# Kernel tuning notes

Hardware: AMD Instinct MI355X
Metric: run time of the kernel (lower is better)

## Reference

```python
import jax, jax.numpy as jnp
import numpy as np
import math

SEQ = 45000
FEAT = 30
DEPTH, HEADS, DK, MLP, C = 4, 4, 32, 512, 32
MAXSEQ = 512


def pos_embed_table():
    # Enformer-style basis functions over distances [-SEQ+1, SEQ-1]
    d = jnp.arange(-SEQ + 1, SEQ, dtype=jnp.float32)
    a = jnp.abs(d)[:, None]
    nb = FEAT // 6  # basis per class (exponential / central-mask / gamma)
    # exponential decay
    hl = 2.0 ** jnp.linspace(3.0, math.log(SEQ) / math.log(2.0), nb)
    e1 = jnp.exp(-math.log(2.0) / hl[None, :] * a)
    # central mask
    cw = 2.0 ** jnp.arange(1, nb + 1, dtype=jnp.float32) - 1.0
    e2 = (cw[None, :] > a).astype(jnp.float32)
    # gamma pdf
    stddev = SEQ / (2 * nb)
    start_mean = SEQ / nb
    mean = jnp.linspace(start_mean, float(SEQ), nb)
    conc = (mean / stddev) ** 2
    rate = mean / stddev ** 2
    logp = jax.scipy.special.xlogy(conc - 1.0, a) - rate * a
    logz = jax.scipy.special.gammaln(conc) - conc * jnp.log(rate)
    p = jnp.exp(logp - logz) + 1e-8
    e3 = p / jnp.max(p)
    e = jnp.concatenate([e1, e2, e3], axis=-1)
    return jnp.concatenate([e, jnp.sign(d)[:, None] * e], axis=-1)  # [2*SEQ-1, FEAT]


def layernorm(x, g, b, eps=1e-5):
    mu = jnp.mean(x, axis=-1, keepdims=True)
    var = jnp.var(x, axis=-1, keepdims=True)
    return (x - mu) * jax.lax.rsqrt(var + eps) * g + b


def setup_inputs() -> dict:
    key = jax.random.key(0)
    ks = jax.random.split(key, 16)
    B, L = 2, SEQ
    HD = HEADS * DK
    s = 0.02
    return {
        "x_skip": jax.random.normal(ks[0], (B, C, L), jnp.float32),
        "attention": jax.random.uniform(ks[1], (B, 3, L), jnp.float32),
        "ln1_g": jnp.ones((DEPTH, C), jnp.float32),
        "ln1_b": jnp.zeros((DEPTH, C), jnp.float32),
        "Wq": jax.random.normal(ks[2], (DEPTH, C, HD), jnp.float32) * s,
        "Wk": jax.random.normal(ks[3], (DEPTH, C, HD), jnp.float32) * s,
        "Wv": jax.random.normal(ks[4], (DEPTH, C, HD), jnp.float32) * s,
        "Wrel": jax.random.normal(ks[5], (DEPTH, FEAT, HD), jnp.float32) * s,
        "rcb": jax.random.normal(ks[6], (DEPTH, HEADS, DK), jnp.float32),
        "rpb": jax.random.normal(ks[7], (DEPTH, HEADS, DK), jnp.float32),
        "Wo": jax.random.normal(ks[8], (DEPTH, HD, C), jnp.float32) * s,
        "bo": jnp.zeros((DEPTH, C), jnp.float32),
        "ln2_g": jnp.ones((DEPTH, C), jnp.float32),
        "ln2_b": jnp.zeros((DEPTH, C), jnp.float32),
        "W1": jax.random.normal(ks[9], (DEPTH, C, MLP), jnp.float32) * s,
        "b1": jnp.zeros((DEPTH, MLP), jnp.float32),
        "W2": jax.random.normal(ks[10], (DEPTH, MLP, C), jnp.float32) * s,
        "b2": jnp.zeros((DEPTH, C), jnp.float32),
    }


def reference(x_skip, attention, ln1_g, ln1_b, Wq, Wk, Wv, Wrel, rcb, rpb, Wo, bo, ln2_g, ln2_b, W1, b1, W2, b2):
    B, Cc, L = x_skip.shape
    half = MAXSEQ // 2
    x_emb = jnp.swapaxes(x_skip, 1, 2)  # [B, L, C]
    # top splice sites by acceptor / donor score
    acc = jnp.argsort(-attention[:, 1, :], axis=1)[:, :half]
    don = jnp.argsort(-attention[:, 2, :], axis=1)[:, :half]
    idx = jnp.sort(jnp.concatenate([acc, don], axis=1), axis=1)  # [B, n]
    n = idx.shape[1]
    diff = idx[:, :, None] - idx[:, None, :] + SEQ - 1  # [B, n, n]
    positions = pos_embed_table()[diff]  # [B, n, n, FEAT]
    emb = jnp.take_along_axis(x_emb, idx[:, :, None], axis=1)  # [B, n, C]
    scale = DK ** -0.5
    for l in range(DEPTH):
        h = layernorm(emb, ln1_g[l], ln1_b[l])
        q = (h @ Wq[l]).reshape(B, n, HEADS, DK).transpose(0, 2, 1, 3) * scale
        k = (h @ Wk[l]).reshape(B, n, HEADS, DK).transpose(0, 2, 1, 3)
        v = (h @ Wv[l]).reshape(B, n, HEADS, DK).transpose(0, 2, 1, 3)
        content = jnp.einsum('bhid,bhjd->bhij', q + rcb[l][None, :, None, :], k)
        rel_k = (positions @ Wrel[l]).reshape(B, n, n, HEADS, DK)  # b i j h d
        rel = jnp.einsum('bhid,bijhd->bhij', q + rpb[l][None, :, None, :], rel_k)
        attn_w = jax.nn.softmax(content + rel, axis=-1)
        o = jnp.einsum('bhij,bhjd->bhid', attn_w, v)
        o = o.transpose(0, 2, 1, 3).reshape(B, n, HEADS * DK)
        emb = emb + o @ Wo[l] + bo[l]
        h2 = layernorm(emb, ln2_g[l], ln2_b[l])
        emb = emb + jax.nn.gelu(h2 @ W1[l] + b1[l], approximate=False) @ W2[l] + b2[l]
    out = jnp.zeros_like(x_emb).at[jnp.arange(B)[:, None], idx].set(emb)
    return jnp.swapaxes(out, 1, 2)  # [B, C, L]
```

## Files before the change

### kernel.cpp

```cpp
#include <hip/hip_runtime.h>
#include <math.h>

#define SEQL   45000
#define NBAT   2
#define CCH    32
#define NSEL   512
#define NHEAD  4
#define DKD    32
#define HDD    128
#define MLPD   512
#define CDCAP  2048
#define ETB    176

__device__ __forceinline__ unsigned short f2bf(float x) {
  unsigned u = __float_as_uint(x);
  u = (u + 0x7fffu + ((u >> 16) & 1u)) >> 16;
  return (unsigned short)u;
}
#define BFL(u) __uint_as_float((u) << 16)
#define BFH(u) __uint_as_float((u) & 0xffff0000u)
#define U8F(w, s) ((float)(((w) >> (s)) & 0xffu))

__global__ __launch_bounds__(256) void prep_kernel(unsigned char* __restrict__ E,
                                                   float* __restrict__ out) {
  {
    int nthr = gridDim.x * 256;
    int gt = blockIdx.x * 256 + threadIdx.x;
    float4 z4 = make_float4(0.f, 0.f, 0.f, 0.f);
    float4* o4 = (float4*)out;
    for (int i = gt; i < NBAT * CCH * SEQL / 4; i += nthr) o4[i] = z4;
  }
  if (blockIdx.x >= ETB) return;
  int a = blockIdx.x * 256 + threadIdx.x;
  if (a >= SEQL) return;
  float ad = (float)a;
  float outv[16];
  float log2S = log2f((float)SEQL);
  #pragma unroll
  for (int k = 0; k < 5; ++k) {
    float hl = exp2f(3.0f + (float)k * (log2S - 3.0f) * 0.25f);
    outv[k] = exp2f(-ad / hl);
  }
  const int cw[5] = {1, 3, 7, 15, 31};
  #pragma unroll
  for (int k = 0; k < 5; ++k) outv[5 + k] = (a < cw[k]) ? 1.0f : 0.0f;
  float pmax = 0.0f;
  float pk[5];
  #pragma unroll
  for (int k = 0; k < 5; ++k) {
    float mean = 9000.0f * (float)(k + 1);
    float sd = 4500.0f;
    float cc = (mean / sd) * (mean / sd);
    float rr = mean / (sd * sd);
    float logz = lgammaf(cc) - cc * logf(rr);
    float pp;
    if (a == 0) pp = 1e-8f;
    else pp = expf((cc - 1.0f) * logf(ad) - rr * ad - logz) + 1e-8f;
    pk[k] = pp;
    float mstar = (cc - 1.0f) / rr;
    float m0 = floorf(mstar), m1 = m0 + 1.0f;
    if (m1 > (float)(SEQL - 1)) m1 = (float)(SEQL - 1);
    float p0 = expf((cc - 1.0f) * logf(m0) - rr * m0 - logz) + 1e-8f;
    float p1 = expf((cc - 1.0f) * logf(m1) - rr * m1 - logz) + 1e-8f;
    pmax = fmaxf(pmax, fmaxf(p0, p1));
  }
  #pragma unroll
  for (int k = 0; k < 5; ++k) outv[10 + k] = pk[k] / pmax;
  outv[15] = 0.0f;
  unsigned by[16];
  #pragma unroll
  for (int k = 0; k < 15; ++k)
    by[k] = (unsigned)(fminf(fmaxf(outv[k], 0.f), 1.f) * 255.f + 0.5f);
  by[15] = 0u;
  uint4 o;
  o.x = by[0]  | (by[1]  << 8) | (by[2]  << 16) | (by[3]  << 24);
  o.y = by[4]  | (by[5]  << 8) | (by[6]  << 16) | (by[7]  << 24);
  o.z = by[8]  | (by[9]  << 8) | (by[10] << 16) | (by[11] << 24);
  o.w = by[12] | (by[13] << 8) | (by[14] << 16);
  *(uint4*)(E + (size_t)a * 16) = o;
}

__global__ __launch_bounds__(1024) void topk_channel_kernel(
    const float* __restrict__ att, unsigned* __restrict__ chsel) {
  __shared__ unsigned long long sc[CDCAP];
  __shared__ int hist[256];
  __shared__ int scan[256];
  __shared__ int aux[2];
  __shared__ int cnt;
  int ch4 = blockIdx.x, t = threadIdx.x;
  int b = ch4 >> 1, ch = ch4 & 1;
  const float* row = att + ((size_t)b * 3 + 1 + ch) * SEQL;
  if (t < 256) hist[t] = 0;
  if (t == 0) cnt = 0;
  __syncthreads();
  for (int i = t; i < SEQL; i += 1024)
    atomicAdd(&hist[__float_as_uint(row[i]) >> 24], 1);
  __syncthreads();
  if (t < 256) scan[t] = hist[t];
  __syncthreads();
  for (int d = 1; d < 256; d <<= 1) {
    int v = 0;
    if (t < 256) v = scan[t] + ((t + d < 256) ? scan[t + d] : 0);
    __syncthreads();
    if (t < 256) scan[t] = v;
    __syncthreads();
  }
  if (t < 256) {
    int sufEx = (t == 255) ? 0 : scan[t + 1];
    if (scan[t] >= 256 && sufEx < 256) { aux[0] = t; aux[1] = 256 - sufEx; }
  }
  __syncthreads();
  int B = aux[0], want = aux[1];
  if (t < 256) hist[t] = 0;
  __syncthreads();
  for (int i = t; i < SEQL; i += 1024) {
    unsigned key = __float_as_uint(row[i]);
    if ((int)(key >> 24) == B) atomicAdd(&hist[(key >> 16) & 0xffu], 1);
  }
  __syncthreads();
  if (t < 256) scan[t] = hist[t];
  __syncthreads();
  for (int d = 1; d < 256; d <<= 1) {
    int v = 0;
    if (t < 256) v = scan[t] + ((t + d < 256) ? scan[t + d] : 0);
    __syncthreads();
    if (t < 256) scan[t] = v;
    __syncthreads();
  }
  if (t < 256) {
    int sufEx = (t == 255) ? 0 : scan[t + 1];
    if (scan[t] >= want && sufEx < want) aux[0] = (B << 8) | t;
  }
  __syncthreads();
  unsigned T16 = (unsigned)aux[0];
  for (int i = t; i < SEQL; i += 1024) {
    unsigned key = __float_as_uint(row[i]);
    if ((key >> 16) >= T16) {
      int p = atomicAdd(&cnt, 1);
      if (p < CDCAP)
        sc[p] = ((unsigned long long)key << 32) | (unsigned)(~(unsigned)i);
    }
  }
  __syncthreads();
  int n = cnt; if (n > CDCAP) n = CDCAP;
  int P = 256;
  while (P < n) P <<= 1;
  for (int i2 = t; i2 < P; i2 += 1024)
    if (i2 >= n) sc[i2] = 0ull;
  __syncthreads();
  for (int k = 2; k <= P; k <<= 1) {
    for (int j = k >> 1; j > 0; j >>= 1) {
      for (int i2 = t; i2 < P; i2 += 1024) {
        int ixj = i2 ^ j;
        if (ixj > i2) {
          unsigned long long va = sc[i2], vb2 = sc[ixj];
          bool up = ((i2 & k) == 0);
          if ((va < vb2) == up) { sc[i2] = vb2; sc[ixj] = va; }
        }
      }
      __syncthreads();
    }
  }
  if (t < 256)
    chsel[(size_t)ch4 * 256 + t] = ~(unsigned)(sc[t] & 0xFFFFFFFFull);
}

__global__ __launch_bounds__(512) void topk_merge_kernel(const unsigned* __restrict__ chsel,
                                                         int* __restrict__ idx) {
  __shared__ int m[512];
  int b = blockIdx.x, tid = threadIdx.x;
  m[tid] = (int)chsel[(size_t)b * 512 + tid];
  __syncthreads();
  for (int k = 2; k <= 512; k <<= 1) {
    for (int j = k >> 1; j > 0; j >>= 1) {
      int ixj = tid ^ j;
      if (ixj > tid) {
        int va = m[tid], vb2 = m[ixj];
        bool up = ((tid & k) == 0);
        if ((va > vb2) == up) { m[tid] = vb2; m[ixj] = va; }
      }
      __syncthreads();
    }
  }
  idx[b * 512 + tid] = m[tid];
}

__global__ __launch_bounds__(128) void gqkv0_kernel(
    const float* __restrict__ x, const int* __restrict__ idx,
    const float* __restrict__ ln_g, const float* __restrict__ ln_b,
    const float* __restrict__ Wq, const float* __restrict__ Wk,
    const float* __restrict__ Wv, const float* __restrict__ Wrel,
    const float* __restrict__ rcb, const float* __restrict__ rpb,
    float* __restrict__ emb, float* __restrict__ qc,
    unsigned short* __restrict__ kbT, unsigned short* __restrict__ vT,
    float* __restrict__ wb) {
  __shared__ float qs[128];
  const int l = 0;
  int hd = threadIdx.x;
  int hh = hd >> 5, d = hd & 31;
  int row = blockIdx.x;
  int b = row >> 9, ii = row & 511;
  int li = idx[b * NSEL + ii];
  float h[32];
  float mu = 0.f;
  #pragma unroll
  for (int c = 0; c < 32; ++c) {
    h[c] = x[((size_t)b * CCH + c) * SEQL + li];
    mu += h[c];
  }
  if (hd < 32) emb[(size_t)row * CCH + hd] = h[hd];
  mu *= (1.0f / 32.0f);
  float var = 0.f;
  #pragma unroll
  for (int c = 0; c < 32; ++c) { float dd0 = h[c] - mu; var += dd0 * dd0; }
  var *= (1.0f / 32.0f);
  float rstd = rsqrtf(var + 1e-5f);
  const float* g = ln_g + l * CCH;
  const float* bb = ln_b + l * CCH;
  #pragma unroll
  for (int c = 0; c < 32; ++c) h[c] = (h[c] - mu) * rstd * g[c] + bb[c];
  const float* wq = Wq + (size_t)l * CCH * HDD + hd;
  const float* wk = Wk + (size_t)l * CCH * HDD + hd;
  const float* wv = Wv + (size_t)l * CCH * HDD + hd;
  float q = 0.f, kk = 0.f, vv = 0.f;
  #pragma unroll
  for (int c = 0; c < 32; ++c) {
    q += h[c] * wq[c * HDD];
    kk += h[c] * wk[c * HDD];
    vv += h[c] * wv[c * HDD];
  }
  q *= 0.17677669529663687f;
  qs[hd] = q;
  qc[(size_t)row * HDD + hd] = q + rcb[(l * NHEAD + hh) * DKD + d];
  size_t tpos = ((size_t)(b * 4 + hh) * 4 + (d >> 3)) * 4096 + (size_t)ii * 8 + (d & 7);
  kbT[tpos] = f2bf(kk);
  vT[tpos]  = f2bf(vv);
  __syncthreads();
  if (hd < 120) {
    int h2 = hd / 30, f = hd % 30;
    const float* wr = Wrel + ((size_t)l * 30 + f) * HDD + h2 * DKD;
    const float* rp = rpb + (l * NHEAD + h2) * DKD;
    const float* qsh = qs + h2 * DKD;
    float acc = 0.f;
    #pragma unroll
    for (int dd = 0; dd < 32; ++dd) acc += (qsh[dd] + rp[dd]) * wr[dd];
    wb[((size_t)row * NHEAD + h2) * 32 + f] = acc;
  }
}

__global__ __launch_bounds__(256, 4) void layer_kernel(
    const float* __restrict__ qc, const unsigned short* __restrict__ kbT,
    const unsigned short* __restrict__ vT, const float* __restrict__ wbuf,
    const unsigned char* __restrict__ E, const int* __restrict__ idx,
    const float* __restrict__ Wo, const float* __restrict__ bo,
    const float* __restrict__ ln2_g, const float* __restrict__ ln2_b,
    const float* __restrict__ W1, const float* __restrict__ b1,
    const float* __restrict__ W2, const float* __restrict__ b2,
    const float* __restrict__ ln1_g, const float* __restrict__ ln1_b,
    const float* __restrict__ Wq, const float* __restrict__ Wk,
    const float* __restrict__ Wv, const float* __restrict__ Wrel,
    const float* __restrict__ rcb, const float* __restrict__ rpb,
    float* __restrict__ emb, float* __restrict__ qcN,
    unsigned short* __restrict__ kbTN, unsigned short* __restrict__ vTN,
    float* __restrict__ wbN, float* __restrict__ out, int layer) {
  __shared__ float2 es2[8 * 512];
  __shared__ float obs[128];
  __shared__ float part[8][32];
  __shared__ float res[32];
  __shared__ float hln[32];
  __shared__ float fin[32];
  __shared__ float a1s[MLPD];
  __shared__ float qs[128];
  int bid = blockIdx.x;
  int b = bid >> 9;
  int i = bid & 511;
  int tid = threadIdx.x;
  int pos = idx[b * NSEL + i];
  #pragma unroll
  for (int rep = 0; rep < 2; ++rep) {
    int j = tid + rep * 256;
    int dj = pos - idx[b * NSEL + j];
    int a = dj < 0 ? -dj : dj;
    uint4 e = *(const uint4*)(E + (size_t)a * 16);
    float sgn = dj > 0 ? 1.f : (dj < 0 ? -1.f : 0.f);
    es2[0 * 512 + j] = make_float2(U8F(e.x, 0),  U8F(e.x, 8));
    es2[1 * 512 + j] = make_float2(U8F(e.x, 16), U8F(e.x, 24));
    es2[2 * 512 + j] = make_float2(U8F(e.y, 0),  U8F(e.y, 8));
    es2[3 * 512 + j] = make_float2(U8F(e.y, 16), U8F(e.y, 24));
    es2[4 * 512 + j] = make_float2(U8F(e.z, 0),  U8F(e.z, 8));
    es2[5 * 512 + j] = make_float2(U8F(e.z, 16), U8F(e.z, 24));
    es2[6 * 512 + j] = make_float2(U8F(e.w, 0),  U8F(e.w, 8));
    es2[7 * 512 + j] = make_float2(U8F(e.w, 16), sgn);
  }
  __syncthreads();
  {
    int h = tid >> 6, ln = tid & 63;
    const float* qrow = qc + (size_t)(b * NSEL + i) * HDD + h * DKD;
    float q[32];
    #pragma unroll
    for (int d4 = 0; d4 < 8; ++d4) {
      float4 qv = *(const float4*)(qrow + d4 * 4);
      q[d4 * 4 + 0] = qv.x; q[d4 * 4 + 1] = qv.y;
      q[d4 * 4 + 2] = qv.z; q[d4 * 4 + 3] = qv.w;
    }
    const float* wrow = wbuf + ((size_t)(b * NSEL + i) * NHEAD + h) * 32;
    float w0[15], w1[15];
    #pragma unroll
    for (int f = 0; f < 15; ++f) {
      w0[f] = wrow[f] * (1.0f / 255.0f);
      w1[f] = wrow[15 + f] * (1.0f / 255.0f);
    }
    const uint4* kb4 = (const uint4*)kbT + (size_t)(b * 4 + h) * 4 * 512;
    const uint4* vb4 = (const uint4*)vT + (size_t)(b * 4 + h) * 4 * 512;
    float lg[8];
    #pragma unroll
    for (int u = 0; u < 8; ++u) {
      int j = u * 64 + ln;
      float cacc = 0.f;
      #pragma unroll
      for (int dp = 0; dp < 4; ++dp) {
        uint4 kv = kb4[dp * 512 + j];
        cacc += q[dp * 8 + 0] * BFL(kv.x) + q[dp * 8 + 1] * BFH(kv.x)
              + q[dp * 8 + 2] * BFL(kv.y) + q[dp * 8 + 3] * BFH(kv.y)
              + q[dp * 8 + 4] * BFL(kv.z) + q[dp * 8 + 5] * BFH(kv.z)
              + q[dp * 8 + 6] * BFL(kv.w) + q[dp * 8 + 7] * BFH(kv.w);
      }
      float r0 = 0.f, r1 = 0.f;
      float2 e7 = es2[7 * 512 + j];
      #pragma unroll
      for (int f2 = 0; f2 < 7; ++f2) {
        float2 ee = es2[f2 * 512 + j];
        r0 += ee.x * w0[2 * f2] + ee.y * w0[2 * f2 + 1];
        r1 += ee.x * w1[2 * f2] + ee.y * w1[2 * f2 + 1];
      }
      r0 += e7.x * w0[14];
      r1 += e7.x * w1[14];
      lg[u] = cacc + r0 + e7.y * r1;
    }
    float m = lg[0];
    #pragma unroll
    for (int u = 1; u < 8; ++u) m = fmaxf(m, lg[u]);
    #pragma unroll
    for (int s = 1; s < 64; s <<= 1) m = fmaxf(m, __shfl_xor(m, s));
    float ssum = 0.f;
    #pragma unroll
    for (int u = 0; u < 8; ++u) { lg[u] = __expf(lg[u] - m); ssum += lg[u]; }
    #pragma unroll
    for (int s = 1; s < 64; s <<= 1) ssum += __shfl_xor(ssum, s);
    float invs = 1.0f / ssum;
    #pragma unroll
    for (int dp = 0; dp < 4; ++dp) {
      float acc[8] = {0.f, 0.f, 0.f, 0.f, 0.f, 0.f, 0.f, 0.f};
      #pragma unroll
      for (int u = 0; u < 8; ++u) {
        uint4 vv = vb4[dp * 512 + u * 64 + ln];
        float p = lg[u];
        acc[0] += p * BFL(vv.x); acc[1] += p * BFH(vv.x);
        acc[2] += p * BFL(vv.y); acc[3] += p * BFH(vv.y);
        acc[4] += p * BFL(vv.z); acc[5] += p * BFH(vv.z);
        acc[6] += p * BFL(vv.w); acc[7] += p * BFH(vv.w);
      }
      #pragma unroll
      for (int s = 1; s < 8; s <<= 1) {
        #pragma unroll
        for (int t = 0; t < 8; ++t) acc[t] += __shfl_xor(acc[t], s);
      }
      int sel = ln & 7;
      float y = acc[0];
      #pragma unroll
      for (int t = 1; t < 8; ++t) y = (sel == t) ? acc[t] : y;
      #pragma unroll
      for (int s = 8; s < 64; s <<= 1) y += __shfl_xor(y, s);
      if (ln < 8) obs[h * DKD + dp * 8 + ln] = y * invs;
    }
  }
  __syncthreads();
  int c = tid & 31, seg = tid >> 5;
  {
    const float* wo = Wo + (size_t)layer * HDD * CCH + c;
    float pacc = 0.f;
    #pragma unroll
    for (int k = 0; k < 16; ++k) {
      int kk = seg * 16 + k;
      pacc += obs[kk] * wo[kk * CCH];
    }
    part[seg][c] = pacc;
  }
  __syncthreads();
  if (tid < 32) {
    float s = bo[layer * CCH + tid] + emb[(size_t)bid * CCH + tid];
    #pragma unroll
    for (int sg = 0; sg < 8; ++sg) s += part[sg][tid];
    res[tid] = s;
  }
  __syncthreads();
  if (tid < 32) {
    float mu = 0.f, s2 = 0.f;
    #pragma unroll
    for (int c2 = 0; c2 < 32; ++c2) { float v = res[c2]; mu += v; s2 += v * v; }
    mu *= (1.0f / 32.0f);
    float var = s2 * (1.0f / 32.0f) - mu * mu;
    float rstd = rsqrtf(var + 1e-5f);
    hln[tid] = (res[tid] - mu) * rstd * ln2_g[layer * CCH + tid] + ln2_b[layer * CCH + tid];
  }
  __syncthreads();
  {
    const float* w1 = W1 + (size_t)layer * CCH * MLPD;
    float accA = b1[layer * MLPD + tid];
    float accB = b1[layer * MLPD + tid + 256];
    for (int c2 = 0; c2 < 32; ++c2) {
      float hv = hln[c2];
      accA += hv * w1[c2 * MLPD + tid];
      accB += hv * w1[c2 * MLPD + tid + 256];
    }
    a1s[tid]       = 0.5f * accA * (1.0f + erff(accA * 0.70710678118654752f));
    a1s[tid + 256] = 0.5f * accB * (1.0f + erff(accB * 0.70710678118654752f));
  }
  __syncthreads();
  {
    const float* w2 = W2 + (size_t)layer * MLPD * CCH;
    float acc2 = 0.f;
    #pragma unroll 4
    for (int mi = 0; mi < 64; ++mi) {
      int m = seg * 64 + mi;
      acc2 += a1s[m] * w2[m * CCH + c];
    }
    __syncthreads();
    part[seg][c] = acc2;
  }
  __syncthreads();
  if (tid < 32) {
    float s = b2[layer * CCH + tid] + res[tid];
    #pragma unroll
    for (int sg = 0; sg < 8; ++sg) s += part[sg][tid];
    fin[tid] = s;
    if (layer < 3) emb[(size_t)bid * CCH + tid] = s;
  }
  __syncthreads();
  if (layer == 3) {
    if (tid < 32) out[((size_t)b * CCH + tid) * SEQL + pos] = fin[tid];
    return;
  }
  const int l1 = layer + 1;
  bool act = tid < 128;
  int hd = tid & 127;
  int hh2 = hd >> 5, dd2 = hd & 31;
  if (act) {
    float hx[32];
    float mu = 0.f;
    #pragma unroll
    for (int c2 = 0; c2 < 32; ++c2) { hx[c2] = fin[c2]; mu += hx[c2]; }
    mu *= (1.0f / 32.0f);
    float var = 0.f;
    #pragma unroll
    for (int c2 = 0; c2 < 32; ++c2) { float dd = hx[c2] - mu; var += dd * dd; }
    var *= (1.0f / 32.0f);
    float rstd = rsqrtf(var + 1e-5f);
    const float* g = ln1_g + l1 * CCH;
    const float* bb = ln1_b + l1 * CCH;
    #pragma unroll
    for (int c2 = 0; c2 < 32; ++c2) hx[c2] = (hx[c2] - mu) * rstd * g[c2] + bb[c2];
    const float* wq = Wq + (size_t)l1 * CCH * HDD + hd;
    const float* wk = Wk + (size_t)l1 * CCH * HDD + hd;
    const float* wv = Wv + (size_t)l1 * CCH * HDD + hd;
    float q = 0.f, kk = 0.f, vv = 0.f;
    #pragma unroll
    for (int c2 = 0; c2 < 32; ++c2) {
      q += hx[c2] * wq[c2 * HDD];
      kk += hx[c2] * wk[c2 * HDD];
      vv += hx[c2] * wv[c2 * HDD];
    }
    q *= 0.17677669529663687f;
    qs[hd] = q;
    qcN[(size_t)bid * HDD + hd] = q + rcb[(l1 * NHEAD + hh2) * DKD + dd2];
    size_t tpos = ((size_t)(b * 4 + hh2) * 4 + (dd2 >> 3)) * 4096 + (size_t)i * 8 + (dd2 & 7);
    kbTN[tpos] = f2bf(kk);
    vTN[tpos]  = f2bf(vv);
  }
  __syncthreads();
  if (act && hd < 120) {
    int h2 = hd / 30, f = hd % 30;
    const float* rp = rpb + (l1 * NHEAD + h2) * DKD;
    const float* wr = Wrel + ((size_t)l1 * 30 + f) * HDD + h2 * DKD;
    const float* qsh = qs + h2 * DKD;
    float acc = 0.f;
    #pragma unroll
    for (int dd = 0; dd < 32; ++dd) acc += (qsh[dd] + rp[dd]) * wr[dd];
    wbN[((size_t)bid * NHEAD + h2) * 32 + f] = acc;
  }
}

extern "C" void kernel_launch(void* const* d_in, const int* in_sizes, int n_in,
                              void* d_out, int out_size, void* d_ws, size_t ws_size,
                              hipStream_t stream) {
  (void)in_sizes; (void)n_in; (void)ws_size; (void)out_size;
  const float* x_skip    = (const float*)d_in[0];
  const float* attention = (const float*)d_in[1];
  const float* ln1_g = (const float*)d_in[2];
  const float* ln1_b = (const float*)d_in[3];
  const float* Wq    = (const float*)d_in[4];
  const float* Wk    = (const float*)d_in[5];
  const float* Wv    = (const float*)d_in[6];
  const float* Wrel  = (const float*)d_in[7];
  const float* rcb   = (const float*)d_in[8];
  const float* rpb   = (const float*)d_in[9];
  const float* Wo    = (const float*)d_in[10];
  const float* bo    = (const float*)d_in[11];
  const float* ln2_g = (const float*)d_in[12];
  const float* ln2_b = (const float*)d_in[13];
  const float* W1    = (const float*)d_in[14];
  const float* b1    = (const float*)d_in[15];
  const float* W2    = (const float*)d_in[16];
  const float* b2    = (const float*)d_in[17];
  float* out = (float*)d_out;
  char* ws = (char*)d_ws;

  unsigned char* E = (unsigned char*)(ws + 0);
  int*      idx   = (int*)(ws + 1441792);
  float*    emb   = (float*)(ws + 1445888);
  float*    qcA   = (float*)(ws + 1576960);
  unsigned short* kbTA = (unsigned short*)(ws + 2101248);
  unsigned short* vTA  = (unsigned short*)(ws + 2363392);
  float*    wbA   = (float*)(ws + 2625536);
  unsigned short* kbTB = (unsigned short*)(ws + 3149824);
  unsigned short* vTB  = (unsigned short*)(ws + 3411968);
  unsigned* chsel = (unsigned*)(ws + 4788256);
  float*    qcB   = (float*)(ws + 4792352);
  float*    wbB   = (float*)(ws + 5316640);

  prep_kernel<<<ETB + 128, 256, 0, stream>>>(attention ? E : E, out);
  topk_channel_kernel<<<4, 1024, 0, stream>>>(attention, chsel);
  topk_merge_kernel<<<2, 512, 0, stream>>>(chsel, idx);
  gqkv0_kernel<<<1024, 128, 0, stream>>>(x_skip, idx, ln1_g, ln1_b, Wq, Wk, Wv,
                                         Wrel, rcb, rpb, emb, qcA, kbTA, vTA, wbA);
  for (int l = 0; l < 4; ++l) {
    const float* qcI = (l & 1) ? qcB : qcA;
    const unsigned short* kbI = (l & 1) ? kbTB : kbTA;
    const unsigned short* vI  = (l & 1) ? vTB : vTA;
    const float* wbI = (l & 1) ? wbB : wbA;
    float* qcO = (l & 1) ? qcA : qcB;
    unsigned short* kbO = (l & 1) ? kbTA : kbTB;
    unsigned short* vO  = (l & 1) ? vTA : vTB;
    float* wbO = (l & 1) ? wbA : wbB;
    layer_kernel<<<1024, 256, 0, stream>>>(qcI, kbI, vI, wbI, E, idx,
                                           Wo, bo, ln2_g, ln2_b, W1, b1, W2, b2,
                                           ln1_g, ln1_b, Wq, Wk, Wv, Wrel, rcb,
                                           rpb, emb, qcO, kbO, vO, wbO, out, l);
  }
}
```

Measured before the change: 300.6 us.

## Parallelize radix top-k selection across many blocks with global histograms

Replaces the four-block top-k kernel, where each block scans a whole 45000-element row three times, with a multi-pass scheme across 128 blocks. Each row is split into 32 slices. The first-byte histogram is fused into the prep kernel, the second-byte histogram gets its own kernel, and candidate collection uses wave-ballot compaction into a global buffer. A final per-channel bitonic sort then runs on the candidates. This trades extra kernel launches, a memset and global atomics for much wider parallelism on the serial selection phase.

```diff
diff --git a/kernel.cpp b/kernel.cpp
--- a/kernel.cpp
+++ b/kernel.cpp
@@ -10,6 +10,7 @@
 #define HDD    128
 #define MLPD   512
 #define CDCAP  2048
+#define NSLICE 32
 #define ETB    176
 
 __device__ __forceinline__ unsigned short f2bf(float x) {
@@ -21,8 +22,11 @@
 #define BFH(u) __uint_as_float((u) & 0xffff0000u)
 #define U8F(w, s) ((float)(((w) >> (s)) & 0xffu))
 
-__global__ __launch_bounds__(256) void prep_kernel(unsigned char* __restrict__ E,
+__global__ __launch_bounds__(256) void prep_kernel(const float* __restrict__ att,
+                                                   unsigned char* __restrict__ E,
+                                                   int* __restrict__ ghist1,
                                                    float* __restrict__ out) {
+  __shared__ int lh[256];
   {
     int nthr = gridDim.x * 256;
     int gt = blockIdx.x * 256 + threadIdx.x;
@@ -30,132 +34,197 @@
     float4* o4 = (float4*)out;
     for (int i = gt; i < NBAT * CCH * SEQL / 4; i += nthr) o4[i] = z4;
   }
-  if (blockIdx.x >= ETB) return;
-  int a = blockIdx.x * 256 + threadIdx.x;
-  if (a >= SEQL) return;
-  float ad = (float)a;
-  float outv[16];
-  float log2S = log2f((float)SEQL);
-  #pragma unroll
-  for (int k = 0; k < 5; ++k) {
-    float hl = exp2f(3.0f + (float)k * (log2S - 3.0f) * 0.25f);
-    outv[k] = exp2f(-ad / hl);
-  }
-  const int cw[5] = {1, 3, 7, 15, 31};
-  #pragma unroll
-  for (int k = 0; k < 5; ++k) outv[5 + k] = (a < cw[k]) ? 1.0f : 0.0f;
-  float pmax = 0.0f;
-  float pk[5];
-  #pragma unroll
-  for (int k = 0; k < 5; ++k) {
-    float mean = 9000.0f * (float)(k + 1);
-    float sd = 4500.0f;
-    float cc = (mean / sd) * (mean / sd);
-    float rr = mean / (sd * sd);
-    float logz = lgammaf(cc) - cc * logf(rr);
-    float pp;
-    if (a == 0) pp = 1e-8f;
-    else pp = expf((cc - 1.0f) * logf(ad) - rr * ad - logz) + 1e-8f;
-    pk[k] = pp;
-    float mstar = (cc - 1.0f) / rr;
-    float m0 = floorf(mstar), m1 = m0 + 1.0f;
-    if (m1 > (float)(SEQL - 1)) m1 = (float)(SEQL - 1);
-    float p0 = expf((cc - 1.0f) * logf(m0) - rr * m0 - logz) + 1e-8f;
-    float p1 = expf((cc - 1.0f) * logf(m1) - rr * m1 - logz) + 1e-8f;
-    pmax = fmaxf(pmax, fmaxf(p0, p1));
-  }
-  #pragma unroll
-  for (int k = 0; k < 5; ++k) outv[10 + k] = pk[k] / pmax;
-  outv[15] = 0.0f;
-  unsigned by[16];
-  #pragma unroll
-  for (int k = 0; k < 15; ++k)
-    by[k] = (unsigned)(fminf(fmaxf(outv[k], 0.f), 1.f) * 255.f + 0.5f);
-  by[15] = 0u;
-  uint4 o;
-  o.x = by[0]  | (by[1]  << 8) | (by[2]  << 16) | (by[3]  << 24);
-  o.y = by[4]  | (by[5]  << 8) | (by[6]  << 16) | (by[7]  << 24);
-  o.z = by[8]  | (by[9]  << 8) | (by[10] << 16) | (by[11] << 24);
-  o.w = by[12] | (by[13] << 8) | (by[14] << 16);
-  *(uint4*)(E + (size_t)a * 16) = o;
-}
-
-__global__ __launch_bounds__(1024) void topk_channel_kernel(
-    const float* __restrict__ att, unsigned* __restrict__ chsel) {
-  __shared__ unsigned long long sc[CDCAP];
-  __shared__ int hist[256];
+  if (blockIdx.x < ETB) {
+    int a = blockIdx.x * 256 + threadIdx.x;
+    if (a >= SEQL) return;
+    float ad = (float)a;
+    float outv[16];
+    float log2S = log2f((float)SEQL);
+    #pragma unroll
+    for (int k = 0; k < 5; ++k) {
+      float hl = exp2f(3.0f + (float)k * (log2S - 3.0f) * 0.25f);
+      outv[k] = exp2f(-ad / hl);
+    }
+    const int cw[5] = {1, 3, 7, 15, 31};
+    #pragma unroll
+    for (int k = 0; k < 5; ++k) outv[5 + k] = (a < cw[k]) ? 1.0f : 0.0f;
+    float pmax = 0.0f;
+    float pk[5];
+    #pragma unroll
+    for (int k = 0; k < 5; ++k) {
+      float mean = 9000.0f * (float)(k + 1);
+      float sd = 4500.0f;
+      float cc = (mean / sd) * (mean / sd);
+      float rr = mean / (sd * sd);
+      float logz = lgammaf(cc) - cc * logf(rr);
+      float pp;
+      if (a == 0) pp = 1e-8f;
+      else pp = expf((cc - 1.0f) * logf(ad) - rr * ad - logz) + 1e-8f;
+      pk[k] = pp;
+      float mstar = (cc - 1.0f) / rr;
+      float m0 = floorf(mstar), m1 = m0 + 1.0f;
+      if (m1 > (float)(SEQL - 1)) m1 = (float)(SEQL - 1);
+      float p0 = expf((cc - 1.0f) * logf(m0) - rr * m0 - logz) + 1e-8f;
+      float p1 = expf((cc - 1.0f) * logf(m1) - rr * m1 - logz) + 1e-8f;
+      pmax = fmaxf(pmax, fmaxf(p0, p1));
+    }
+    #pragma unroll
+    for (int k = 0; k < 5; ++k) outv[10 + k] = pk[k] / pmax;
+    outv[15] = 0.0f;
+    unsigned by[16];
+    #pragma unroll
+    for (int k = 0; k < 15; ++k)
+      by[k] = (unsigned)(fminf(fmaxf(outv[k], 0.f), 1.f) * 255.f + 0.5f);
+    by[15] = 0u;
+    uint4 o;
+    o.x = by[0]  | (by[1]  << 8) | (by[2]  << 16) | (by[3]  << 24);
+    o.y = by[4]  | (by[5]  << 8) | (by[6]  << 16) | (by[7]  << 24);
+    o.z = by[8]  | (by[9]  << 8) | (by[10] << 16) | (by[11] << 24);
+    o.w = by[12] | (by[13] << 8) | (by[14] << 16);
+    *(uint4*)(E + (size_t)a * 16) = o;
+  } else {
+    int bid = blockIdx.x - ETB;
+    int ch4 = bid >> 5, blk = bid & 31;
+    int b = ch4 >> 1, ch = ch4 & 1;
+    const float* row = att + ((size_t)b * 3 + 1 + ch) * SEQL;
+    int t = threadIdx.x;
+    lh[t] = 0;
+    __syncthreads();
+    int per = (SEQL + NSLICE - 1) / NSLICE;
+    int lo = blk * per;
+    int hi = lo + per; if (hi > SEQL) hi = SEQL;
+    for (int i = lo + t; i < hi; i += 256)
+      atomicAdd(&lh[__float_as_uint(row[i]) >> 24], 1);
+    __syncthreads();
+    if (lh[t]) atomicAdd(&ghist1[ch4 * 256 + t], lh[t]);
+  }
+}
+
+__global__ __launch_bounds__(256) void topk_hist2_kernel(
+    const float* __restrict__ att, const int* __restrict__ ghist1,
+    int* __restrict__ ghist2) {
+  __shared__ int scan[256];
+  __shared__ int lh[256];
+  __shared__ int auxB;
+  int bid = blockIdx.x;
+  int ch4 = bid >> 5, blk = bid & 31;
+  int b = ch4 >> 1, ch = ch4 & 1;
+  const float* row = att + ((size_t)b * 3 + 1 + ch) * SEQL;
+  int t = threadIdx.x;
+  scan[t] = ghist1[ch4 * 256 + t];
+  __syncthreads();
+  for (int d = 1; d < 256; d <<= 1) {
+    int v = scan[t] + ((t + d < 256) ? scan[t + d] : 0);
+    __syncthreads();
+    scan[t] = v;
+    __syncthreads();
+  }
+  {
+    int sufEx = (t == 255) ? 0 : scan[t + 1];
+    if (scan[t] >= 256 && sufEx < 256) auxB = t;
+  }
+  __syncthreads();
+  int B = auxB;
+  lh[t] = 0;
+  __syncthreads();
+  int per = (SEQL + NSLICE - 1) / NSLICE;
+  int lo = blk * per;
+  int hi = lo + per; if (hi > SEQL) hi = SEQL;
+  for (int i = lo + t; i < hi; i += 256) {
+    unsigned key = __float_as_uint(row[i]);
+    if ((int)(key >> 24) == B) atomicAdd(&lh[(key >> 16) & 0xffu], 1);
+  }
+  __syncthreads();
+  if (lh[t]) atomicAdd(&ghist2[ch4 * 256 + t], lh[t]);
+}
+
+__global__ __launch_bounds__(256) void topk_collect_kernel(
+    const float* __restrict__ att, const int* __restrict__ ghist1,
+    const int* __restrict__ ghist2, unsigned long long* __restrict__ cand,
+    int* __restrict__ cnt) {
   __shared__ int scan[256];
   __shared__ int aux[2];
-  __shared__ int cnt;
-  int ch4 = blockIdx.x, t = threadIdx.x;
+  int bid = blockIdx.x;
+  int ch4 = bid >> 5, blk = bid & 31;
   int b = ch4 >> 1, ch = ch4 & 1;
   const float* row = att + ((size_t)b * 3 + 1 + ch) * SEQL;
-  if (t < 256) hist[t] = 0;
-  if (t == 0) cnt = 0;
-  __syncthreads();
-  for (int i = t; i < SEQL; i += 1024)
-    atomicAdd(&hist[__float_as_uint(row[i]) >> 24], 1);
-  __syncthreads();
-  if (t < 256) scan[t] = hist[t];
+  int t = threadIdx.x;
+  scan[t] = ghist1[ch4 * 256 + t];
   __syncthreads();
   for (int d = 1; d < 256; d <<= 1) {
-    int v = 0;
-    if (t < 256) v = scan[t] + ((t + d < 256) ? scan[t + d] : 0);
-    __syncthreads();
-    if (t < 256) scan[t] = v;
-    __syncthreads();
-  }
-  if (t < 256) {
+    int v = scan[t] + ((t + d < 256) ? scan[t + d] : 0);
+    __syncthreads();
+    scan[t] = v;
+    __syncthreads();
+  }
+  {
     int sufEx = (t == 255) ? 0 : scan[t + 1];
     if (scan[t] >= 256 && sufEx < 256) { aux[0] = t; aux[1] = 256 - sufEx; }
   }
   __syncthreads();
   int B = aux[0], want = aux[1];
-  if (t < 256) hist[t] = 0;
-  __syncthreads();
-  for (int i = t; i < SEQL; i += 1024) {
-    unsigned key = __float_as_uint(row[i]);
-    if ((int)(key >> 24) == B) atomicAdd(&hist[(key >> 16) & 0xffu], 1);
-  }
-  __syncthreads();
-  if (t < 256) scan[t] = hist[t];
+  scan[t] = ghist2[ch4 * 256 + t];
   __syncthreads();
   for (int d = 1; d < 256; d <<= 1) {
-    int v = 0;
-    if (t < 256) v = scan[t] + ((t + d < 256) ? scan[t + d] : 0);
-    __syncthreads();
-    if (t < 256) scan[t] = v;
-    __syncthreads();
-  }
-  if (t < 256) {
+    int v = scan[t] + ((t + d < 256) ? scan[t + d] : 0);
+    __syncthreads();
+    scan[t] = v;
+    __syncthreads();
+  }
+  {
     int sufEx = (t == 255) ? 0 : scan[t + 1];
     if (scan[t] >= want && sufEx < want) aux[0] = (B << 8) | t;
   }
   __syncthreads();
   unsigned T16 = (unsigned)aux[0];
-  for (int i = t; i < SEQL; i += 1024) {
-    unsigned key = __float_as_uint(row[i]);
-    if ((key >> 16) >= T16) {
-      int p = atomicAdd(&cnt, 1);
-      if (p < CDCAP)
-        sc[p] = ((unsigned long long)key << 32) | (unsigned)(~(unsigned)i);
-    }
-  }
-  __syncthreads();
-  int n = cnt; if (n > CDCAP) n = CDCAP;
+  int per = (SEQL + NSLICE - 1) / NSLICE;
+  int lo = blk * per;
+  int hi = lo + per; if (hi > SEQL) hi = SEQL;
+  int lane = t & 63;
+  for (int base = lo; base < hi; base += 256) {
+    int i = base + t;
+    bool pass = false; unsigned key = 0;
+    if (i < hi) {
+      key = __float_as_uint(row[i]);
+      pass = (key >> 16) >= T16;
+    }
+    unsigned long long mask = __ballot(pass);
+    if (mask) {
+      int np = __popcll(mask);
+      int lead = __ffsll((long long)mask) - 1;
+      int pbase = 0;
+      if (lane == lead) pbase = atomicAdd(&cnt[ch4], np);
+      pbase = __shfl(pbase, lead);
+      if (pass) {
+        int off = __popcll(mask & ((1ull << lane) - 1ull));
+        int p = pbase + off;
+        if (p < CDCAP)
+          cand[(size_t)ch4 * CDCAP + p] =
+              ((unsigned long long)key << 32) | (unsigned)(~(unsigned)i);
+      }
+    }
+  }
+}
+
+__global__ __launch_bounds__(1024) void topk_sort_kernel(
+    const unsigned long long* __restrict__ cand, const int* __restrict__ cnt,
+    unsigned* __restrict__ chsel) {
+  __shared__ unsigned long long sc[CDCAP];
+  int ch4 = blockIdx.x, t = threadIdx.x;
+  int n = cnt[ch4]; if (n > CDCAP) n = CDCAP;
   int P = 256;
   while (P < n) P <<= 1;
-  for (int i2 = t; i2 < P; i2 += 1024)
-    if (i2 >= n) sc[i2] = 0ull;
+  for (int i = t; i < P; i += 1024)
+    sc[i] = (i < n) ? cand[(size_t)ch4 * CDCAP + i] : 0ull;
   __syncthreads();
   for (int k = 2; k <= P; k <<= 1) {
     for (int j = k >> 1; j > 0; j >>= 1) {
-      for (int i2 = t; i2 < P; i2 += 1024) {
-        int ixj = i2 ^ j;
-        if (ixj > i2) {
-          unsigned long long va = sc[i2], vb2 = sc[ixj];
-          bool up = ((i2 & k) == 0);
-          if ((va < vb2) == up) { sc[i2] = vb2; sc[ixj] = va; }
+      for (int i = t; i < P; i += 1024) {
+        int ixj = i ^ j;
+        if (ixj > i) {
+          unsigned long long va = sc[i], vb2 = sc[ixj];
+          bool up = ((i & k) == 0);
+          if ((va < vb2) == up) { sc[i] = vb2; sc[ixj] = va; }
         }
       }
       __syncthreads();
@@ -524,12 +593,19 @@
   float*    wbA   = (float*)(ws + 2625536);
   unsigned short* kbTB = (unsigned short*)(ws + 3149824);
   unsigned short* vTB  = (unsigned short*)(ws + 3411968);
+  int*      ghist1 = (int*)(ws + 3674112);
+  int*      ghist2 = (int*)(ws + 3678208);
+  int*      cnt    = (int*)(ws + 3682304);
+  unsigned long long* cand = (unsigned long long*)(ws + 4722720);
   unsigned* chsel = (unsigned*)(ws + 4788256);
   float*    qcB   = (float*)(ws + 4792352);
   float*    wbB   = (float*)(ws + 5316640);
 
-  prep_kernel<<<ETB + 128, 256, 0, stream>>>(attention ? E : E, out);
-  topk_channel_kernel<<<4, 1024, 0, stream>>>(attention, chsel);
+  hipMemsetAsync(ws + 3674112, 0, 4096 + 4096 + 32, stream);
+  prep_kernel<<<ETB + 128, 256, 0, stream>>>(attention, E, ghist1, out);
+  topk_hist2_kernel<<<128, 256, 0, stream>>>(attention, ghist1, ghist2);
+  topk_collect_kernel<<<128, 256, 0, stream>>>(attention, ghist1, ghist2, cand, cnt);
+  topk_sort_kernel<<<4, 1024, 0, stream>>>(cand, cnt, chsel);
   topk_merge_kernel<<<2, 512, 0, stream>>>(chsel, idx);
   gqkv0_kernel<<<1024, 128, 0, stream>>>(x_skip, idx, ln1_g, ln1_b, Wq, Wk, Wv,
                                          Wrel, rcb, rpb, emb, qcA, kbTA, vTA, wbA);
```

New measurement: 281.9 us (median of 3 runs). -6.2%, faster.
